# Kernel optimization log

Hardware: AMD Instinct MI355X
Metric: run time of the kernel (lower is better)

## Reference

```python
import jax, jax.numpy as jnp
import numpy as np

B, D, U = 64, 512, 512  # batch, input, units
EPS = 1e-5

def _ln(x, g, b, axes):
    m = jnp.mean(x, axis=axes, keepdims=True)
    v = jnp.mean((x - m) ** 2, axis=axes, keepdims=True)
    return (x - m) * jax.lax.rsqrt(v + EPS) * g + b

def setup_inputs() -> dict:
    key = jax.random.key(0)
    ks = jax.random.split(key, 8)
    w = lambda k, shape: 0.02 * jax.random.normal(k, shape, dtype=jnp.float32)
    return {
        "x": jax.random.normal(ks[0], (B, D), dtype=jnp.float32),
        "w1": w(ks[1], (1, D, U, 2)),
        "b1": jnp.zeros((1, D, U, 2), jnp.float32),
        "w21": w(ks[2], (1, D, U, 2)),
        "w22": w(ks[3], (1, D, U, 2)),
        "b21": jnp.zeros((1, D, U, 1), jnp.float32),
        "b22": jnp.zeros((1, D, U, 1), jnp.float32),
        "w3": w(ks[4], (1, D, U, 2)),
        "b3": jnp.zeros((1, D, U, 1), jnp.float32),
        "bias": jnp.zeros((U,), jnp.float32),
        "g0": jnp.ones((D,), jnp.float32), "be0": jnp.zeros((D,), jnp.float32),
        "g1": jnp.ones((D, U, 2), jnp.float32), "be1": jnp.zeros((D, U, 2), jnp.float32),
        "g2": jnp.ones((D, U, 2), jnp.float32), "be2": jnp.zeros((D, U, 2), jnp.float32),
        "g3": jnp.ones((D, U, 1), jnp.float32), "be3": jnp.zeros((D, U, 1), jnp.float32),
    }

def reference(x, w1, b1, w21, w22, b21, b22, w3, b3, bias,
              g0, be0, g1, be1, g2, be2, g3, be3):
    lrelu = lambda t: jnp.where(t >= 0, t, 0.01 * t)  # nn.LeakyReLU default slope
    xn = _ln(x, g0, be0, (-1,))[:, :, None, None]           # [B,D,1,1]
    l1 = lrelu(_ln(xn * w1 + b1, g1, be1, (1, 2, 3)))        # [B,D,U,2]
    l21 = jnp.sum(l1 * w21, axis=-1, keepdims=True) + b21    # [B,D,U,1]
    l22 = jnp.sum(l1 * w22, axis=-1, keepdims=True) + b22    # [B,D,U,1]
    l2 = lrelu(_ln(jnp.concatenate((l21, l22), axis=-1), g2, be2, (1, 2, 3)))  # [B,D,U,2]
    l3 = jnp.sum(l2 * w3, axis=-1, keepdims=True) + b3       # [B,D,U,1]
    out = _ln(l3, g3, be3, (1, 2, 3)) + xn                   # [B,D,U,1]
    out = lrelu(jnp.sum(out, axis=1) + bias[:, None])        # [B,U,1]
    return jnp.squeeze(out, axis=-1)                         # [B,U]
```

## Files before the change

kernel.cpp:

```cpp
#include <hip/hip_runtime.h>

#define EPS 1e-5f
constexpr float INV_N1 = 1.f / 524288.f;
constexpr float INV_N3 = 1.f / 262144.f;

__device__ __forceinline__ float lrelu(float y) { return fmaxf(y, 0.01f * y); }

template <int CTRL>
__device__ __forceinline__ float dppMov(float v) {
    return __int_as_float(__builtin_amdgcn_update_dpp(
        0, __float_as_int(v), CTRL, 0xF, 0xF, true));
}
__device__ __forceinline__ float waveSumDpp(float v) {
    v += dppMov<0x111>(v);
    v += dppMov<0x112>(v);
    v += dppMov<0x114>(v);
    v += dppMov<0x118>(v);
    v += dppMov<0x142>(v);
    v += dppMov<0x143>(v);
    return v;
}
__device__ __forceinline__ float quadSum(float v) {
    v += dppMov<0xB1>(v);
    v += dppMov<0x4E>(v);
    return v;
}
__device__ __forceinline__ float waveAllSum(float v) {
    v += __shfl_xor(v, 32); v += __shfl_xor(v, 16); v += __shfl_xor(v, 8);
    v += __shfl_xor(v, 4);  v += __shfl_xor(v, 2);  v += __shfl_xor(v, 1);
    return v;
}

__global__ void __launch_bounds__(256) kA(
    const float* __restrict__ w1, const float* __restrict__ b1,
    const float* __restrict__ g3, const float* __restrict__ be3,
    const float* __restrict__ x, const float* __restrict__ g0,
    const float* __restrict__ be0,
    float* __restrict__ S1, float* __restrict__ S2, float* __restrict__ S11,
    float* __restrict__ S0b, float* __restrict__ Sb2,
    float* __restrict__ Gp, float* __restrict__ Bp,
    float* __restrict__ xn, float* __restrict__ Xs, float* __restrict__ st2) {
    int bid = blockIdx.x, tid = threadIdx.x;
    int wave = tid >> 6, lane = tid & 63;
    __shared__ float red[4][5];
    __shared__ float bc[2];
    if (bid < 512) {
        const float4* wr = (const float4*)(w1 + bid * 1024);
        const float4* br = (const float4*)(b1 + bid * 1024);
        float4 w = wr[tid], b = br[tid];
        float s1  = w.x + w.y + w.z + w.w;
        float s2  = w.x * w.x + w.y * w.y + w.z * w.z + w.w * w.w;
        float s11 = w.x * b.x + w.y * b.y + w.z * b.z + w.w * b.w;
        float s0  = b.x + b.y + b.z + b.w;
        float sb2 = b.x * b.x + b.y * b.y + b.z * b.z + b.w * b.w;
        s1 = waveAllSum(s1); s2 = waveAllSum(s2); s11 = waveAllSum(s11);
        s0 = waveAllSum(s0); sb2 = waveAllSum(sb2);
        if (lane == 0) {
            red[wave][0] = s1; red[wave][1] = s2; red[wave][2] = s11;
            red[wave][3] = s0; red[wave][4] = sb2;
        }
        __syncthreads();
        if (tid == 0) {
            float a0 = 0, a1 = 0, a2 = 0, a3 = 0, a4 = 0;
            for (int w4 = 0; w4 < 4; ++w4) {
                a0 += red[w4][0]; a1 += red[w4][1]; a2 += red[w4][2];
                a3 += red[w4][3]; a4 += red[w4][4];
            }
            S1[bid] = a0; S2[bid] = a1; S11[bid] = a2;
            S0b[bid] = a3; Sb2[bid] = a4;
        }
    } else if (bid < 576) {
        int jj = bid - 512;
        float ag0 = 0, ag1 = 0, ab0 = 0, ab1 = 0;
#pragma unroll
        for (int r = 0; r < 8; ++r) {
            const float* gr = g3 + (jj * 8 + r) * 512;
            const float* br = be3 + (jj * 8 + r) * 512;
            ag0 += gr[tid]; ag1 += gr[tid + 256];
            ab0 += br[tid]; ab1 += br[tid + 256];
        }
        Gp[jj * 512 + tid] = ag0; Gp[jj * 512 + tid + 256] = ag1;
        Bp[jj * 512 + tid] = ab0; Bp[jj * 512 + tid + 256] = ab1;
    } else if (bid < 640) {
        int b = bid - 576;
        float2 xv = ((const float2*)(x + b * 512))[tid];
        float sx = xv.x + xv.y, sxx = xv.x * xv.x + xv.y * xv.y;
        sx = waveAllSum(sx); sxx = waveAllSum(sxx);
        if (lane == 0) { red[wave][0] = sx; red[wave][1] = sxx; }
        __syncthreads();
        if (tid == 0) {
            float s = red[0][0] + red[1][0] + red[2][0] + red[3][0];
            float c = red[0][1] + red[1][1] + red[2][1] + red[3][1];
            float m = s * (1.f / 512.f);
            float var = c * (1.f / 512.f) - m * m;
            bc[0] = m; bc[1] = rsqrtf(var + EPS);
        }
        __syncthreads();
        float m = bc[0], rsd = bc[1];
        float2 g = ((const float2*)g0)[tid], be = ((const float2*)be0)[tid];
        float xn0 = (xv.x - m) * rsd * g.x + be.x;
        float xn1 = (xv.y - m) * rsd * g.y + be.y;
        ((float2*)(xn + b * 512))[tid] = make_float2(xn0, xn1);
        float sxn = waveAllSum(xn0 + xn1);
        __syncthreads();
        if (lane == 0) red[wave][0] = sxn;
        __syncthreads();
        if (tid == 0) Xs[b] = red[0][0] + red[1][0] + red[2][0] + red[3][0];
    } else {
        for (int t = tid; t < 2048; t += 256) st2[t] = 0.f;
    }
}

__global__ void __launch_bounds__(256) kS(
    const float* __restrict__ xn,
    const float* __restrict__ S1, const float* __restrict__ S2,
    const float* __restrict__ S11, const float* __restrict__ S0b,
    const float* __restrict__ Sb2,
    const float* __restrict__ Gp, const float* __restrict__ Bp,
    float* __restrict__ rs1a, float* __restrict__ mm1a,
    float* __restrict__ G3s, float* __restrict__ Be3s) {
    int bid = blockIdx.x, tid = threadIdx.x;
    if (bid < 64) {
        int b = bid;
        __shared__ float red[4][2];
        float2 xv  = ((const float2*)(xn + b * 512))[tid];
        float2 s1  = ((const float2*)S1)[tid],  s0b = ((const float2*)S0b)[tid];
        float2 s2  = ((const float2*)S2)[tid],  s11 = ((const float2*)S11)[tid];
        float2 sb2 = ((const float2*)Sb2)[tid];
        float pm = fmaf(xv.x, s1.x, s0b.x) + fmaf(xv.y, s1.y, s0b.y);
        float pe = xv.x * xv.x * s2.x + 2.f * xv.x * s11.x + sb2.x
                 + xv.y * xv.y * s2.y + 2.f * xv.y * s11.y + sb2.y;
        pm = waveAllSum(pm); pe = waveAllSum(pe);
        int wave = tid >> 6, lane = tid & 63;
        if (lane == 0) { red[wave][0] = pm; red[wave][1] = pe; }
        __syncthreads();
        if (tid == 0) {
            float s = red[0][0] + red[1][0] + red[2][0] + red[3][0];
            float c = red[0][1] + red[1][1] + red[2][1] + red[3][1];
            float m1 = s * INV_N1, e1 = c * INV_N1;
            float r = rsqrtf(e1 - m1 * m1 + EPS);
            rs1a[b] = r; mm1a[b] = m1 * r;
        }
    } else if (bid == 64) {
        for (int u = tid; u < 512; u += 256) {
            float s = 0;
#pragma unroll 8
            for (int jj = 0; jj < 64; ++jj) s += Gp[jj * 512 + u];
            G3s[u] = s;
        }
    } else {
        for (int u = tid; u < 512; u += 256) {
            float s = 0;
#pragma unroll 8
            for (int jj = 0; jj < 64; ++jj) s += Bp[jj * 512 + u];
            Be3s[u] = s;
        }
    }
}

__global__ void __launch_bounds__(256) k1(
    const float* __restrict__ w1, const float* __restrict__ b1,
    const float* __restrict__ g1, const float* __restrict__ be1,
    const float* __restrict__ w21, const float* __restrict__ w22,
    const float* __restrict__ b21, const float* __restrict__ b22,
    const float* __restrict__ xnp, const float* __restrict__ rs1a,
    const float* __restrict__ mm1a, float* __restrict__ st2) {
    int bid = blockIdx.x, tid = threadIdx.x;
    int d = bid >> 1;
    int u = ((bid & 1) << 8) + tid;
    int i = d * 512 + u;
    float2 W1 = ((const float2*)w1)[i], B1 = ((const float2*)b1)[i];
    float2 G1 = ((const float2*)g1)[i], E1 = ((const float2*)be1)[i];
    float2 A = ((const float2*)w21)[i], C = ((const float2*)w22)[i];
    float Ba = b21[i], Bc = b22[i];
    __shared__ float xcol[64], scA[64], scB[64];
    __shared__ float red[64][4][2];
    if (tid < 64) {
        xcol[tid] = xnp[tid * 512 + d];
        scA[tid] = rs1a[tid];
        scB[tid] = mm1a[tid];
    }
    __syncthreads();
    int wave = tid >> 6, lane = tid & 63;
    for (int b = 0; b < 64; ++b) {
        float rs1 = scA[b], mm1 = scB[b], xd = xcol[b];
        float t0 = fmaf(xd, W1.x, B1.x), t1 = fmaf(xd, W1.y, B1.y);
        float z0 = fmaf(t0, rs1, -mm1), z1 = fmaf(t1, rs1, -mm1);
        float y0 = fmaf(z0, G1.x, E1.x), y1 = fmaf(z1, G1.y, E1.y);
        float l0 = lrelu(y0), l1 = lrelu(y1);
        float c0 = fmaf(l0, A.x, fmaf(l1, A.y, Ba));
        float c1 = fmaf(l0, C.x, fmaf(l1, C.y, Bc));
        float v1 = c0 + c1;
        float v2 = fmaf(c0, c0, c1 * c1);
        v1 = waveSumDpp(v1);
        v2 = waveSumDpp(v2);
        if (lane == 63) { red[b][wave][0] = v1; red[b][wave][1] = v2; }
    }
    __syncthreads();
    if (tid < 128) {
        int b = tid >> 1, k = tid & 1;
        float s = red[b][0][k] + red[b][1][k] + red[b][2][k] + red[b][3][k];
        unsafeAtomicAdd(&st2[tid * 16], s);
    }
}

struct Wt { float2 W1, B1, G1, E1, A, C, G2, E2, W3; float Ba, Bc, B3, G3v; };

__global__ void __launch_bounds__(256) k2(
    const float* __restrict__ w1, const float* __restrict__ b1,
    const float* __restrict__ g1, const float* __restrict__ be1,
    const float* __restrict__ w21, const float* __restrict__ w22,
    const float* __restrict__ b21, const float* __restrict__ b22,
    const float* __restrict__ g2, const float* __restrict__ be2,
    const float* __restrict__ w3, const float* __restrict__ b3,
    const float* __restrict__ g3,
    const float* __restrict__ xnp, const float* __restrict__ rs1a,
    const float* __restrict__ mm1a, const float* __restrict__ st2,
    float* __restrict__ pp, float* __restrict__ qp) {
    int bu = blockIdx.x & 31, bd = blockIdx.x >> 5, tid = threadIdx.x;
    int lane = tid & 63, wave = tid >> 6;
    int ul = (lane >> 2) & 15, d0 = lane & 3;
    int u = bu * 16 + ul;
    int dl0 = wave * 8 + d0 * 2;
    Wt wt[2];
#pragma unroll
    for (int j = 0; j < 2; ++j) {
        int d = bd * 32 + dl0 + j;
        int i = d * 512 + u;
        wt[j].W1 = ((const float2*)w1)[i];  wt[j].B1 = ((const float2*)b1)[i];
        wt[j].G1 = ((const float2*)g1)[i];  wt[j].E1 = ((const float2*)be1)[i];
        wt[j].A  = ((const float2*)w21)[i]; wt[j].C  = ((const float2*)w22)[i];
        wt[j].G2 = ((const float2*)g2)[i];  wt[j].E2 = ((const float2*)be2)[i];
        wt[j].W3 = ((const float2*)w3)[i];
        wt[j].Ba = b21[i]; wt[j].Bc = b22[i]; wt[j].B3 = b3[i]; wt[j].G3v = g3[i];
    }
    __shared__ float4 sc[64];
    __shared__ float sxn[64][32];
    __shared__ float comb[4][64][16][3];
    {
        float* cz = &comb[0][0][0][0];
        for (int t = tid; t < 4 * 64 * 16 * 3; t += 256) cz[t] = 0.f;
    }
    if (tid < 64) {
        float ssum = st2[(tid * 2) * 16], s2sum = st2[(tid * 2 + 1) * 16];
        float mm = ssum * INV_N1;
        float var = s2sum * INV_N1 - mm * mm;
        float r2 = rsqrtf(var + EPS);
        sc[tid] = make_float4(rs1a[tid], mm1a[tid], r2, mm * r2);
    }
    for (int idx = tid; idx < 2048; idx += 256)
        sxn[idx >> 5][idx & 31] = xnp[(idx >> 5) * 512 + bd * 32 + (idx & 31)];
    __syncthreads();
    for (int b = 0; b < 64; ++b) {
        float4 s4 = sc[b];
        float p = 0, q = 0, q2 = 0;
#pragma unroll
        for (int j = 0; j < 2; ++j) {
            float xd = sxn[b][dl0 + j];
            float t0 = fmaf(xd, wt[j].W1.x, wt[j].B1.x), t1 = fmaf(xd, wt[j].W1.y, wt[j].B1.y);
            float z0 = fmaf(t0, s4.x, -s4.y), z1 = fmaf(t1, s4.x, -s4.y);
            float y0 = fmaf(z0, wt[j].G1.x, wt[j].E1.x), y1 = fmaf(z1, wt[j].G1.y, wt[j].E1.y);
            float l0 = lrelu(y0), l1 = lrelu(y1);
            float c0 = fmaf(l0, wt[j].A.x, fmaf(l1, wt[j].A.y, wt[j].Ba));
            float c1 = fmaf(l0, wt[j].C.x, fmaf(l1, wt[j].C.y, wt[j].Bc));
            float z20 = fmaf(c0, s4.z, -s4.w), z21 = fmaf(c1, s4.z, -s4.w);
            float y20 = fmaf(z20, wt[j].G2.x, wt[j].E2.x), y21 = fmaf(z21, wt[j].G2.y, wt[j].E2.y);
            float m0 = lrelu(y20), m1v = lrelu(y21);
            float l3 = fmaf(m0, wt[j].W3.x, fmaf(m1v, wt[j].W3.y, wt[j].B3));
            p = fmaf(l3, wt[j].G3v, p); q += l3; q2 = fmaf(l3, l3, q2);
        }
        p = quadSum(p); q = quadSum(q); q2 = quadSum(q2);
        if (d0 < 3) {
            float v = (d0 == 0) ? p : ((d0 == 1) ? q : q2);
            comb[wave][b][ul][d0] += v;
        }
    }
    __syncthreads();
#pragma unroll
    for (int r = 0; r < 4; ++r) {
        int idx = r * 256 + tid;
        int b = idx >> 4, uu = idx & 15;
        float s = comb[0][b][uu][0] + comb[1][b][uu][0]
                + comb[2][b][uu][0] + comb[3][b][uu][0];
        pp[(bd * 64 + b) * 512 + bu * 16 + uu] = s;
    }
    if (tid < 128) {
        int b = tid >> 1, st = 1 + (tid & 1);
        float s = 0;
#pragma unroll
        for (int w = 0; w < 4; ++w)
#pragma unroll
            for (int uu = 0; uu < 16; ++uu) s += comb[w][b][uu][st];
        qp[(bd * 32 + bu) * 128 + b * 2 + (st - 1)] = s;
    }
}

__global__ void __launch_bounds__(512) k3(
    const float* __restrict__ pp, const float* __restrict__ qp,
    const float* __restrict__ G3s, const float* __restrict__ Be3s,
    const float* __restrict__ Xs, const float* __restrict__ bias,
    float* __restrict__ out) {
    int b = blockIdx.x, u = threadIdx.x;
    float q  = qp[u * 128 + b * 2 + 0];
    float q2 = qp[u * 128 + b * 2 + 1];
    __shared__ float red[8][2];
    __shared__ float bc2[2];
    float sq = waveAllSum(q), sq2 = waveAllSum(q2);
    int wave = u >> 6, lane = u & 63;
    if (lane == 0) { red[wave][0] = sq; red[wave][1] = sq2; }
    __syncthreads();
    if (u == 0) {
        float a = 0, c = 0;
        for (int w = 0; w < 8; ++w) { a += red[w][0]; c += red[w][1]; }
        float m3 = a * INV_N3;
        float e3 = c * INV_N3;
        bc2[0] = m3; bc2[1] = rsqrtf(e3 - m3 * m3 + EPS);
    }
    __syncthreads();
    float p = 0;
#pragma unroll 4
    for (int bd = 0; bd < 16; ++bd) p += pp[(bd * 64 + b) * 512 + u];
    float m3 = bc2[0], rs3 = bc2[1];
    float val = rs3 * (p - m3 * G3s[u]) + Be3s[u] + Xs[b] + bias[u];
    out[b * 512 + u] = lrelu(val);
}

extern "C" void kernel_launch(void* const* d_in, const int* in_sizes, int n_in,
                              void* d_out, int out_size, void* d_ws, size_t ws_size,
                              hipStream_t stream) {
    const float* x   = (const float*)d_in[0];
    const float* w1  = (const float*)d_in[1];
    const float* b1  = (const float*)d_in[2];
    const float* w21 = (const float*)d_in[3];
    const float* w22 = (const float*)d_in[4];
    const float* b21 = (const float*)d_in[5];
    const float* b22 = (const float*)d_in[6];
    const float* w3  = (const float*)d_in[7];
    const float* b3  = (const float*)d_in[8];
    const float* bias= (const float*)d_in[9];
    const float* g0  = (const float*)d_in[10];
    const float* be0 = (const float*)d_in[11];
    const float* g1  = (const float*)d_in[12];
    const float* be1 = (const float*)d_in[13];
    const float* g2  = (const float*)d_in[14];
    const float* be2 = (const float*)d_in[15];
    const float* g3  = (const float*)d_in[16];
    const float* be3 = (const float*)d_in[17];
    float* out = (float*)d_out;
    char* ws = (char*)d_ws;

    float* xn   = (float*)(ws);
    float* S1   = (float*)(ws + 131072);
    float* S2   = (float*)(ws + 133120);
    float* S11  = (float*)(ws + 135168);
    float* S0b  = (float*)(ws + 137216);
    float* Sb2  = (float*)(ws + 139264);
    float* rs1a = (float*)(ws + 141312);
    float* mm1a = (float*)(ws + 141568);
    float* Xs   = (float*)(ws + 141824);
    float* st2  = (float*)(ws + 142080);
    float* G3s  = (float*)(ws + 150272);
    float* Be3s = (float*)(ws + 152320);
    float* Gp   = (float*)(ws + 154368);
    float* Bp   = (float*)(ws + 285440);
    float* qp   = (float*)(ws + 416512);
    float* pp   = (float*)(ws + 678656);

    hipLaunchKernelGGL(kA, dim3(641), dim3(256), 0, stream,
                       w1, b1, g3, be3, x, g0, be0,
                       S1, S2, S11, S0b, Sb2, Gp, Bp, xn, Xs, st2);
    hipLaunchKernelGGL(kS, dim3(66), dim3(256), 0, stream,
                       xn, S1, S2, S11, S0b, Sb2, Gp, Bp,
                       rs1a, mm1a, G3s, Be3s);
    hipLaunchKernelGGL(k1, dim3(1024), dim3(256), 0, stream,
                       w1, b1, g1, be1, w21, w22, b21, b22, xn, rs1a, mm1a, st2);
    hipLaunchKernelGGL(k2, dim3(512), dim3(256), 0, stream,
                       w1, b1, g1, be1, w21, w22, b21, b22, g2, be2, w3, b3, g3,
                       xn, rs1a, mm1a, st2, pp, qp);
    hipLaunchKernelGGL(k3, dim3(64), dim3(512), 0, stream,
                       pp, qp, G3s, Be3s, Xs, bias, out);
}
```

Before: 83.29 us.

## Replace atomic stats reduction with per-block partials reduced inside k2

k1 now gives each block a full d row, with two u elements per thread, and writes per-block partial sums to a buffer instead of doing atomicAdd into st2. Every k2 block then re-reduces all 512 partials for its own stats. The x layernorm moves into kB, which lets kA drop its st2 zeroing and split into a simpler weight-stats kernel. Cross-wave reduction now uses row DPP sums with 16-lane partials. This removes atomics and halves k1 blocks, but adds a redundant 256KB partial read in each of the 512 k2 blocks.

```diff
diff --git a/kernel.cpp b/kernel.cpp
--- a/kernel.cpp
+++ b/kernel.cpp
@@ -11,13 +11,11 @@
     return __int_as_float(__builtin_amdgcn_update_dpp(
         0, __float_as_int(v), CTRL, 0xF, 0xF, true));
 }
-__device__ __forceinline__ float waveSumDpp(float v) {
+__device__ __forceinline__ float rowSumDpp(float v) {
     v += dppMov<0x111>(v);
     v += dppMov<0x112>(v);
     v += dppMov<0x114>(v);
     v += dppMov<0x118>(v);
-    v += dppMov<0x142>(v);
-    v += dppMov<0x143>(v);
     return v;
 }
 __device__ __forceinline__ float quadSum(float v) {
@@ -31,19 +29,13 @@
     return v;
 }
 
-__global__ void __launch_bounds__(256) kA(
+__global__ void __launch_bounds__(256) kW(
     const float* __restrict__ w1, const float* __restrict__ b1,
     const float* __restrict__ g3, const float* __restrict__ be3,
-    const float* __restrict__ x, const float* __restrict__ g0,
-    const float* __restrict__ be0,
     float* __restrict__ S1, float* __restrict__ S2, float* __restrict__ S11,
     float* __restrict__ S0b, float* __restrict__ Sb2,
-    float* __restrict__ Gp, float* __restrict__ Bp,
-    float* __restrict__ xn, float* __restrict__ Xs, float* __restrict__ st2) {
+    float* __restrict__ Gp, float* __restrict__ Bp) {
     int bid = blockIdx.x, tid = threadIdx.x;
-    int wave = tid >> 6, lane = tid & 63;
-    __shared__ float red[4][5];
-    __shared__ float bc[2];
     if (bid < 512) {
         const float4* wr = (const float4*)(w1 + bid * 1024);
         const float4* br = (const float4*)(b1 + bid * 1024);
@@ -53,8 +45,10 @@
         float s11 = w.x * b.x + w.y * b.y + w.z * b.z + w.w * b.w;
         float s0  = b.x + b.y + b.z + b.w;
         float sb2 = b.x * b.x + b.y * b.y + b.z * b.z + b.w * b.w;
+        __shared__ float red[4][5];
         s1 = waveAllSum(s1); s2 = waveAllSum(s2); s11 = waveAllSum(s11);
         s0 = waveAllSum(s0); sb2 = waveAllSum(sb2);
+        int wave = tid >> 6, lane = tid & 63;
         if (lane == 0) {
             red[wave][0] = s1; red[wave][1] = s2; red[wave][2] = s11;
             red[wave][3] = s0; red[wave][4] = sb2;
@@ -69,77 +63,75 @@
             S1[bid] = a0; S2[bid] = a1; S11[bid] = a2;
             S0b[bid] = a3; Sb2[bid] = a4;
         }
-    } else if (bid < 576) {
+    } else {
         int jj = bid - 512;
         float ag0 = 0, ag1 = 0, ab0 = 0, ab1 = 0;
 #pragma unroll
         for (int r = 0; r < 8; ++r) {
             const float* gr = g3 + (jj * 8 + r) * 512;
             const float* br = be3 + (jj * 8 + r) * 512;
-            ag0 += gr[tid]; ag1 += gr[tid + 256];
-            ab0 += br[tid]; ab1 += br[tid + 256];
+            ag0 += gr[tid];  ag1 += gr[tid + 256];
+            ab0 += br[tid];  ab1 += br[tid + 256];
         }
         Gp[jj * 512 + tid] = ag0; Gp[jj * 512 + tid + 256] = ag1;
         Bp[jj * 512 + tid] = ab0; Bp[jj * 512 + tid + 256] = ab1;
-    } else if (bid < 640) {
-        int b = bid - 576;
-        float2 xv = ((const float2*)(x + b * 512))[tid];
-        float sx = xv.x + xv.y, sxx = xv.x * xv.x + xv.y * xv.y;
-        sx = waveAllSum(sx); sxx = waveAllSum(sxx);
-        if (lane == 0) { red[wave][0] = sx; red[wave][1] = sxx; }
-        __syncthreads();
-        if (tid == 0) {
-            float s = red[0][0] + red[1][0] + red[2][0] + red[3][0];
-            float c = red[0][1] + red[1][1] + red[2][1] + red[3][1];
-            float m = s * (1.f / 512.f);
-            float var = c * (1.f / 512.f) - m * m;
-            bc[0] = m; bc[1] = rsqrtf(var + EPS);
-        }
-        __syncthreads();
-        float m = bc[0], rsd = bc[1];
-        float2 g = ((const float2*)g0)[tid], be = ((const float2*)be0)[tid];
-        float xn0 = (xv.x - m) * rsd * g.x + be.x;
-        float xn1 = (xv.y - m) * rsd * g.y + be.y;
-        ((float2*)(xn + b * 512))[tid] = make_float2(xn0, xn1);
-        float sxn = waveAllSum(xn0 + xn1);
-        __syncthreads();
-        if (lane == 0) red[wave][0] = sxn;
-        __syncthreads();
-        if (tid == 0) Xs[b] = red[0][0] + red[1][0] + red[2][0] + red[3][0];
-    } else {
-        for (int t = tid; t < 2048; t += 256) st2[t] = 0.f;
-    }
-}
-
-__global__ void __launch_bounds__(256) kS(
-    const float* __restrict__ xn,
+    }
+}
+
+__global__ void __launch_bounds__(256) kB(
+    const float* __restrict__ x, const float* __restrict__ g0,
+    const float* __restrict__ be0,
     const float* __restrict__ S1, const float* __restrict__ S2,
     const float* __restrict__ S11, const float* __restrict__ S0b,
     const float* __restrict__ Sb2,
     const float* __restrict__ Gp, const float* __restrict__ Bp,
-    float* __restrict__ rs1a, float* __restrict__ mm1a,
-    float* __restrict__ G3s, float* __restrict__ Be3s) {
+    float* __restrict__ xnp, float* __restrict__ rs1a, float* __restrict__ mm1a,
+    float* __restrict__ Xs, float* __restrict__ G3s, float* __restrict__ Be3s) {
     int bid = blockIdx.x, tid = threadIdx.x;
     if (bid < 64) {
         int b = bid;
-        __shared__ float red[4][2];
-        float2 xv  = ((const float2*)(xn + b * 512))[tid];
-        float2 s1  = ((const float2*)S1)[tid],  s0b = ((const float2*)S0b)[tid];
-        float2 s2  = ((const float2*)S2)[tid],  s11 = ((const float2*)S11)[tid];
-        float2 sb2 = ((const float2*)Sb2)[tid];
-        float pm = fmaf(xv.x, s1.x, s0b.x) + fmaf(xv.y, s1.y, s0b.y);
-        float pe = xv.x * xv.x * s2.x + 2.f * xv.x * s11.x + sb2.x
-                 + xv.y * xv.y * s2.y + 2.f * xv.y * s11.y + sb2.y;
-        pm = waveAllSum(pm); pe = waveAllSum(pe);
+        float2 xv = ((const float2*)(x + b * 512))[tid];
+        float sx = xv.x + xv.y;
+        float sxx = xv.x * xv.x + xv.y * xv.y;
+        __shared__ float red[4][3];
+        __shared__ float bc[2];
+        sx = waveAllSum(sx); sxx = waveAllSum(sxx);
         int wave = tid >> 6, lane = tid & 63;
-        if (lane == 0) { red[wave][0] = pm; red[wave][1] = pe; }
+        if (lane == 0) { red[wave][0] = sx; red[wave][1] = sxx; }
         __syncthreads();
         if (tid == 0) {
-            float s = red[0][0] + red[1][0] + red[2][0] + red[3][0];
+            float a = red[0][0] + red[1][0] + red[2][0] + red[3][0];
             float c = red[0][1] + red[1][1] + red[2][1] + red[3][1];
-            float m1 = s * INV_N1, e1 = c * INV_N1;
+            float m = a * (1.f / 512.f);
+            float var = c * (1.f / 512.f) - m * m;
+            bc[0] = m; bc[1] = rsqrtf(var + EPS);
+        }
+        __syncthreads();
+        float m = bc[0], rsd = bc[1];
+        float2 g = ((const float2*)g0)[tid];
+        float2 be = ((const float2*)be0)[tid];
+        float xn0 = (xv.x - m) * rsd * g.x + be.x;
+        float xn1 = (xv.y - m) * rsd * g.y + be.y;
+        ((float2*)(xnp + b * 512))[tid] = make_float2(xn0, xn1);
+        float2 s1 = ((const float2*)S1)[tid], s0b = ((const float2*)S0b)[tid];
+        float2 s2 = ((const float2*)S2)[tid], s11 = ((const float2*)S11)[tid];
+        float2 sb2 = ((const float2*)Sb2)[tid];
+        float pm = fmaf(xn0, s1.x, s0b.x) + fmaf(xn1, s1.y, s0b.y);
+        float pe = xn0 * xn0 * s2.x + 2.f * xn0 * s11.x + sb2.x
+                 + xn1 * xn1 * s2.y + 2.f * xn1 * s11.y + sb2.y;
+        float sxn = xn0 + xn1;
+        pm = waveAllSum(pm); pe = waveAllSum(pe); sxn = waveAllSum(sxn);
+        __syncthreads();
+        if (lane == 0) { red[wave][0] = pm; red[wave][1] = pe; red[wave][2] = sxn; }
+        __syncthreads();
+        if (tid == 0) {
+            float a = red[0][0] + red[1][0] + red[2][0] + red[3][0];
+            float c = red[0][1] + red[1][1] + red[2][1] + red[3][1];
+            float s = red[0][2] + red[1][2] + red[2][2] + red[3][2];
+            float m1 = a * INV_N1;
+            float e1 = c * INV_N1;
             float r = rsqrtf(e1 - m1 * m1 + EPS);
-            rs1a[b] = r; mm1a[b] = m1 * r;
+            rs1a[b] = r; mm1a[b] = m1 * r; Xs[b] = s;
         }
     } else if (bid == 64) {
         for (int u = tid; u < 512; u += 256) {
@@ -164,43 +156,60 @@
     const float* __restrict__ w21, const float* __restrict__ w22,
     const float* __restrict__ b21, const float* __restrict__ b22,
     const float* __restrict__ xnp, const float* __restrict__ rs1a,
-    const float* __restrict__ mm1a, float* __restrict__ st2) {
+    const float* __restrict__ mm1a, float* __restrict__ part1) {
     int bid = blockIdx.x, tid = threadIdx.x;
-    int d = bid >> 1;
-    int u = ((bid & 1) << 8) + tid;
-    int i = d * 512 + u;
-    float2 W1 = ((const float2*)w1)[i], B1 = ((const float2*)b1)[i];
-    float2 G1 = ((const float2*)g1)[i], E1 = ((const float2*)be1)[i];
-    float2 A = ((const float2*)w21)[i], C = ((const float2*)w22)[i];
-    float Ba = b21[i], Bc = b22[i];
+    int d = bid;
     __shared__ float xcol[64], scA[64], scB[64];
-    __shared__ float red[64][4][2];
+    __shared__ float2 red2[64][4][4];
     if (tid < 64) {
         xcol[tid] = xnp[tid * 512 + d];
         scA[tid] = rs1a[tid];
         scB[tid] = mm1a[tid];
     }
+    int i0 = d * 512 + tid, i1 = i0 + 256;
+    float2 W1a = ((const float2*)w1)[i0], B1a = ((const float2*)b1)[i0];
+    float2 G1a = ((const float2*)g1)[i0], E1a = ((const float2*)be1)[i0];
+    float2 Aa  = ((const float2*)w21)[i0], Ca = ((const float2*)w22)[i0];
+    float Baa = b21[i0], Bca = b22[i0];
+    float2 W1b = ((const float2*)w1)[i1], B1b = ((const float2*)b1)[i1];
+    float2 G1b = ((const float2*)g1)[i1], E1b = ((const float2*)be1)[i1];
+    float2 Ab  = ((const float2*)w21)[i1], Cb = ((const float2*)w22)[i1];
+    float Bab = b21[i1], Bcb = b22[i1];
     __syncthreads();
     int wave = tid >> 6, lane = tid & 63;
     for (int b = 0; b < 64; ++b) {
-        float rs1 = scA[b], mm1 = scB[b], xd = xcol[b];
-        float t0 = fmaf(xd, W1.x, B1.x), t1 = fmaf(xd, W1.y, B1.y);
-        float z0 = fmaf(t0, rs1, -mm1), z1 = fmaf(t1, rs1, -mm1);
-        float y0 = fmaf(z0, G1.x, E1.x), y1 = fmaf(z1, G1.y, E1.y);
+        float xd = xcol[b], r1 = scA[b], mmv = scB[b];
+        float t0 = fmaf(xd, W1a.x, B1a.x), t1 = fmaf(xd, W1a.y, B1a.y);
+        float z0 = fmaf(t0, r1, -mmv), z1 = fmaf(t1, r1, -mmv);
+        float y0 = fmaf(z0, G1a.x, E1a.x), y1 = fmaf(z1, G1a.y, E1a.y);
         float l0 = lrelu(y0), l1 = lrelu(y1);
-        float c0 = fmaf(l0, A.x, fmaf(l1, A.y, Ba));
-        float c1 = fmaf(l0, C.x, fmaf(l1, C.y, Bc));
+        float c0 = fmaf(l0, Aa.x, fmaf(l1, Aa.y, Baa));
+        float c1 = fmaf(l0, Ca.x, fmaf(l1, Ca.y, Bca));
         float v1 = c0 + c1;
         float v2 = fmaf(c0, c0, c1 * c1);
-        v1 = waveSumDpp(v1);
-        v2 = waveSumDpp(v2);
-        if (lane == 63) { red[b][wave][0] = v1; red[b][wave][1] = v2; }
+        t0 = fmaf(xd, W1b.x, B1b.x); t1 = fmaf(xd, W1b.y, B1b.y);
+        z0 = fmaf(t0, r1, -mmv); z1 = fmaf(t1, r1, -mmv);
+        y0 = fmaf(z0, G1b.x, E1b.x); y1 = fmaf(z1, G1b.y, E1b.y);
+        l0 = lrelu(y0); l1 = lrelu(y1);
+        c0 = fmaf(l0, Ab.x, fmaf(l1, Ab.y, Bab));
+        c1 = fmaf(l0, Cb.x, fmaf(l1, Cb.y, Bcb));
+        v1 += c0 + c1;
+        v2 = fmaf(c0, c0, fmaf(c1, c1, v2));
+        v1 = rowSumDpp(v1);
+        v2 = rowSumDpp(v2);
+        if ((lane & 15) == 15)
+            red2[b][wave][lane >> 4] = make_float2(v1, v2);
     }
     __syncthreads();
     if (tid < 128) {
         int b = tid >> 1, k = tid & 1;
-        float s = red[b][0][k] + red[b][1][k] + red[b][2][k] + red[b][3][k];
-        unsafeAtomicAdd(&st2[tid * 16], s);
+        float s = 0;
+#pragma unroll
+        for (int w = 0; w < 4; ++w)
+#pragma unroll
+            for (int r = 0; r < 4; ++r)
+                s += ((const float*)&red2[b][w][r])[k];
+        part1[bid * 128 + tid] = s;
     }
 }
 
@@ -215,13 +224,31 @@
     const float* __restrict__ w3, const float* __restrict__ b3,
     const float* __restrict__ g3,
     const float* __restrict__ xnp, const float* __restrict__ rs1a,
-    const float* __restrict__ mm1a, const float* __restrict__ st2,
+    const float* __restrict__ mm1a, const float* __restrict__ part1,
     float* __restrict__ pp, float* __restrict__ qp) {
     int bu = blockIdx.x & 31, bd = blockIdx.x >> 5, tid = threadIdx.x;
     int lane = tid & 63, wave = tid >> 6;
     int ul = (lane >> 2) & 15, d0 = lane & 3;
     int u = bu * 16 + ul;
     int dl0 = wave * 8 + d0 * 2;
+    __shared__ float4 sc[64];
+    __shared__ float sxn[64][32];
+    __shared__ float comb[4][64][16][3];
+    __shared__ float tmp2[2][128];
+    {
+        int s = tid & 127, half = tid >> 7;
+        float acc = 0;
+        const float* p = part1 + half * 256 * 128 + s;
+#pragma unroll 8
+        for (int blk = 0; blk < 256; ++blk) acc += p[blk * 128];
+        tmp2[half][s] = acc;
+    }
+    {
+        float* cz = &comb[0][0][0][0];
+        for (int t = tid; t < 4 * 64 * 16 * 3; t += 256) cz[t] = 0.f;
+    }
+    for (int idx = tid; idx < 2048; idx += 256)
+        sxn[idx >> 5][idx & 31] = xnp[(idx >> 5) * 512 + bd * 32 + (idx & 31)];
     Wt wt[2];
 #pragma unroll
     for (int j = 0; j < 2; ++j) {
@@ -234,22 +261,15 @@
         wt[j].W3 = ((const float2*)w3)[i];
         wt[j].Ba = b21[i]; wt[j].Bc = b22[i]; wt[j].B3 = b3[i]; wt[j].G3v = g3[i];
     }
-    __shared__ float4 sc[64];
-    __shared__ float sxn[64][32];
-    __shared__ float comb[4][64][16][3];
-    {
-        float* cz = &comb[0][0][0][0];
-        for (int t = tid; t < 4 * 64 * 16 * 3; t += 256) cz[t] = 0.f;
-    }
+    __syncthreads();
     if (tid < 64) {
-        float ssum = st2[(tid * 2) * 16], s2sum = st2[(tid * 2 + 1) * 16];
+        float ssum = tmp2[0][2 * tid] + tmp2[1][2 * tid];
+        float s2sum = tmp2[0][2 * tid + 1] + tmp2[1][2 * tid + 1];
         float mm = ssum * INV_N1;
         float var = s2sum * INV_N1 - mm * mm;
         float r2 = rsqrtf(var + EPS);
         sc[tid] = make_float4(rs1a[tid], mm1a[tid], r2, mm * r2);
     }
-    for (int idx = tid; idx < 2048; idx += 256)
-        sxn[idx >> 5][idx & 31] = xnp[(idx >> 5) * 512 + bd * 32 + (idx & 31)];
     __syncthreads();
     for (int b = 0; b < 64; ++b) {
         float4 s4 = sc[b];
@@ -349,34 +369,33 @@
     float* out = (float*)d_out;
     char* ws = (char*)d_ws;
 
-    float* xn   = (float*)(ws);
-    float* S1   = (float*)(ws + 131072);
-    float* S2   = (float*)(ws + 133120);
-    float* S11  = (float*)(ws + 135168);
-    float* S0b  = (float*)(ws + 137216);
-    float* Sb2  = (float*)(ws + 139264);
-    float* rs1a = (float*)(ws + 141312);
-    float* mm1a = (float*)(ws + 141568);
-    float* Xs   = (float*)(ws + 141824);
-    float* st2  = (float*)(ws + 142080);
-    float* G3s  = (float*)(ws + 150272);
-    float* Be3s = (float*)(ws + 152320);
-    float* Gp   = (float*)(ws + 154368);
-    float* Bp   = (float*)(ws + 285440);
-    float* qp   = (float*)(ws + 416512);
-    float* pp   = (float*)(ws + 678656);
-
-    hipLaunchKernelGGL(kA, dim3(641), dim3(256), 0, stream,
-                       w1, b1, g3, be3, x, g0, be0,
-                       S1, S2, S11, S0b, Sb2, Gp, Bp, xn, Xs, st2);
-    hipLaunchKernelGGL(kS, dim3(66), dim3(256), 0, stream,
-                       xn, S1, S2, S11, S0b, Sb2, Gp, Bp,
-                       rs1a, mm1a, G3s, Be3s);
-    hipLaunchKernelGGL(k1, dim3(1024), dim3(256), 0, stream,
-                       w1, b1, g1, be1, w21, w22, b21, b22, xn, rs1a, mm1a, st2);
+    float* xn    = (float*)(ws);
+    float* S1    = (float*)(ws + 131072);
+    float* S2    = (float*)(ws + 133120);
+    float* S11   = (float*)(ws + 135168);
+    float* S0b   = (float*)(ws + 137216);
+    float* Sb2   = (float*)(ws + 139264);
+    float* rs1a  = (float*)(ws + 141312);
+    float* mm1a  = (float*)(ws + 141568);
+    float* Xs    = (float*)(ws + 141824);
+    float* G3s   = (float*)(ws + 142080);
+    float* Be3s  = (float*)(ws + 144128);
+    float* Gp    = (float*)(ws + 146176);
+    float* Bp    = (float*)(ws + 277248);
+    float* part1 = (float*)(ws + 408320);
+    float* qp    = (float*)(ws + 670464);
+    float* pp    = (float*)(ws + 932608);
+
+    hipLaunchKernelGGL(kW, dim3(576), dim3(256), 0, stream,
+                       w1, b1, g3, be3, S1, S2, S11, S0b, Sb2, Gp, Bp);
+    hipLaunchKernelGGL(kB, dim3(66), dim3(256), 0, stream,
+                       x, g0, be0, S1, S2, S11, S0b, Sb2, Gp, Bp,
+                       xn, rs1a, mm1a, Xs, G3s, Be3s);
+    hipLaunchKernelGGL(k1, dim3(512), dim3(256), 0, stream,
+                       w1, b1, g1, be1, w21, w22, b21, b22, xn, rs1a, mm1a, part1);
     hipLaunchKernelGGL(k2, dim3(512), dim3(256), 0, stream,
                        w1, b1, g1, be1, w21, w22, b21, b22, g2, be2, w3, b3, g3,
-                       xn, rs1a, mm1a, st2, pp, qp);
+                       xn, rs1a, mm1a, part1, pp, qp);
     hipLaunchKernelGGL(k3, dim3(64), dim3(512), 0, stream,
                        pp, qp, G3s, Be3s, Xs, bias, out);
 }
```

Result: faster. 72.10 us (-13.4%).
